# Kernel tuning notes

Measured on AMD Instinct MI355X. Metric: run time of the kernel, lower is better.

## Reference

```python
import jax, jax.numpy as jnp
import numpy as np


def _gcn_conv(x, W, b, src, dst, num_nodes):
    # PyG GCNConv: h = x @ W; symmetric normalization with self-loops; scatter-add; + bias
    h = x @ W
    deg = jax.ops.segment_sum(jnp.ones_like(dst, dtype=h.dtype), dst, num_segments=num_nodes)
    dinv = jnp.where(deg > 0, jax.lax.rsqrt(deg), 0.0)
    norm = dinv[src] * dinv[dst]                         # [E]
    msgs = h[src] * norm[:, None]                        # [E, H] gather + scale
    out = jax.ops.segment_sum(msgs, dst, num_segments=num_nodes)
    return out + b


def setup_inputs() -> dict:
    key = jax.random.key(0)
    ks = jax.random.split(key, 10)
    N, E = 500000, 1000000
    IN, H, SIG = 3, 64, 24
    x = jax.random.uniform(ks[0], (N, IN), dtype=jnp.float32)
    edge_index = jax.random.randint(ks[1], (2, E), 0, N, dtype=jnp.int64)
    batch = jnp.zeros((N,), dtype=jnp.int64)
    def glorot(k, shape):
        lim = np.sqrt(6.0 / (shape[0] + shape[1]))
        return jax.random.uniform(k, shape, dtype=jnp.float32, minval=-lim, maxval=lim)
    return {
        "x": x,
        "edge_index": edge_index,
        "batch": batch,
        "W1": glorot(ks[2], (IN, H)), "b1": jnp.zeros((H,), jnp.float32),
        "W2": glorot(ks[3], (H, H)),  "b2": jnp.zeros((H,), jnp.float32),
        "W3": glorot(ks[4], (H, H)),  "b3": jnp.zeros((H,), jnp.float32),
        "Wfc": glorot(ks[5], (H, SIG)), "bfc": jnp.zeros((SIG,), jnp.float32),
    }


def reference(x, edge_index, batch, W1, b1, W2, b2, W3, b3, Wfc, bfc):
    N = x.shape[0]
    NUM_GRAPHS = 1  # batch is all zeros (single graph)
    # add self-loops once (GCNConv adds them per layer; identical edge set each layer)
    loop = jnp.arange(N, dtype=edge_index.dtype)
    src = jnp.concatenate([edge_index[0], loop])
    dst = jnp.concatenate([edge_index[1], loop])

    h = jax.nn.relu(_gcn_conv(x, W1, b1, src, dst, N))
    h = jax.nn.relu(_gcn_conv(h, W2, b2, src, dst, N))
    h = jax.nn.relu(_gcn_conv(h, W3, b3, src, dst, N))

    # global mean pool per graph
    sums = jax.ops.segment_sum(h, batch, num_segments=NUM_GRAPHS)          # [G, H]
    counts = jax.ops.segment_sum(jnp.ones((N,), h.dtype), batch, num_segments=NUM_GRAPHS)
    sig = sums / jnp.maximum(counts, 1.0)[:, None]

    return jnp.tanh(sig @ Wfc + bfc)  # [G, 24]
```

## Files before the change

### kernel.cpp

```cpp
#include <hip/hip_runtime.h>
#include <hip/hip_bf16.h>
#include <hip/hip_fp16.h>


#define ALIGN256(x) (((x) + 255) & ~(size_t)255)
#define NBUCK_MAX 512

typedef _Float16 half8 __attribute__((ext_vector_type(8)));
typedef float f32x4 __attribute__((ext_vector_type(4)));
typedef int i32x4 __attribute__((ext_vector_type(4)));

__device__ __forceinline__ void dec16(i32x4 r, half8& a, half8& b) {
    i32x4 u, v;
    u.x = (int)(((unsigned)r.x << 8) & 0xFF00FF00u);
    u.y = (int)(((unsigned)r.x)      & 0xFF00FF00u);
    u.z = (int)(((unsigned)r.y << 8) & 0xFF00FF00u);
    u.w = (int)(((unsigned)r.y)      & 0xFF00FF00u);
    v.x = (int)(((unsigned)r.z << 8) & 0xFF00FF00u);
    v.y = (int)(((unsigned)r.z)      & 0xFF00FF00u);
    v.z = (int)(((unsigned)r.w << 8) & 0xFF00FF00u);
    v.w = (int)(((unsigned)r.w)      & 0xFF00FF00u);
    a = *(half8*)&u; b = *(half8*)&v;
}

__device__ __forceinline__ unsigned char enc8(float x) {
    unsigned short hb = __half_as_ushort(__float2half(x));
    return (unsigned char)((hb + 0x80u) >> 8);
}

__global__ __launch_bounds__(256) void init_kernel(float* __restrict__ pool, float4* __restrict__ xs,
                                                   unsigned char* __restrict__ h8a,
                                                   unsigned char* __restrict__ h8b, int N) {
    int i = threadIdx.x;
    if (i < 64) pool[i] = 0.f;
    if (i < 16) {
        ((int*)(h8a + (size_t)N * 64))[i] = 0;
        ((int*)(h8b + (size_t)N * 64))[i] = 0;
    }
    if (i == 0) xs[N] = make_float4(0.f, 0.f, 0.f, 0.f);
}

__global__ __launch_bounds__(256) void hist_kernel(const int* __restrict__ ei, int E, int CE, int SH,
                                                   int* __restrict__ cnt_mat) {
    __shared__ int h[NBUCK_MAX];
    const int t = threadIdx.x, blk = blockIdx.x;
    for (int i = t; i < NBUCK_MAX; i += 256) h[i] = 0;
    __syncthreads();
    const int e0 = blk * CE, e1 = min(E, e0 + CE);
    for (int e = e0 + t; e < e1; e += 256)
        atomicAdd(&h[ei[E + e] >> SH], 1);
    __syncthreads();
    for (int i = t; i < NBUCK_MAX; i += 256) cnt_mat[blk * NBUCK_MAX + i] = h[i];
}

__global__ __launch_bounds__(64) void colscan_kernel(const int* __restrict__ cnt_mat,
                                                     int* __restrict__ base_mat,
                                                     int* __restrict__ tot, int nblk) {
    __shared__ int ls[64];
    const int j = blockIdx.x;
    const int t = threadIdx.x;
    const int PER = (nblk + 63) >> 6;
    const int b0 = t * PER, b1 = min(nblk, b0 + PER);
    int s = 0;
    for (int b = b0; b < b1; ++b) s += cnt_mat[b * NBUCK_MAX + j];
    ls[t] = s;
    __syncthreads();
    if (t == 0) {
        int run = 0;
        for (int k = 0; k < 64; ++k) { int v = ls[k]; ls[k] = run; run += v; }
        tot[j] = run;
    }
    __syncthreads();
    int run = ls[t];
    for (int b = b0; b < b1; ++b) {
        int v = cnt_mat[b * NBUCK_MAX + j];
        base_mat[b * NBUCK_MAX + j] = run;
        run += v;
    }
}

__global__ __launch_bounds__(256) void totscan_kernel(const int* __restrict__ tot,
                                                      int* __restrict__ start, int NBK) {
    __shared__ int ls[256];
    const int t = threadIdx.x;
    const int PER = (NBK + 255) >> 8;
    const int j0 = t * PER, j1 = min(NBK, j0 + PER);
    int s = 0;
    for (int j = j0; j < j1; ++j) s += tot[j];
    ls[t] = s;
    __syncthreads();
    if (t == 0) {
        int run = 0;
        for (int k = 0; k < 256; ++k) { int v = ls[k]; ls[k] = run; run += v; }
    }
    __syncthreads();
    int run = ls[t];
    for (int j = j0; j < j1; ++j) { start[j] = run; run += tot[j]; }
}

__global__ __launch_bounds__(256) void scatter_kernel(const int* __restrict__ ei, int E, int CE, int SH,
                                                      const int* __restrict__ base_mat,
                                                      const int* __restrict__ start,
                                                      unsigned* __restrict__ bkt) {
    __shared__ int cur[NBUCK_MAX];
    const int t = threadIdx.x, blk = blockIdx.x;
    for (int i = t; i < NBUCK_MAX; i += 256) cur[i] = 0;
    __syncthreads();
    const int e0 = blk * CE, e1 = min(E, e0 + CE);
    const unsigned lowm = (1u << SH) - 1u;
    for (int e = e0 + t; e < e1; e += 256) {
        int s = ei[e], d = ei[E + e];
        int b = d >> SH;
        int r = atomicAdd(&cur[b], 1);
        int dest = start[b] + base_mat[blk * NBUCK_MAX + b] + r;
        bkt[dest] = (((unsigned)d & lowm) << 21) | (unsigned)s;
    }
}

__global__ __launch_bounds__(256) void build_kernel(const unsigned* __restrict__ bkt,
                                                    const int* __restrict__ start, const int* __restrict__ tot,
                                                    int SH, int nrows,
                                                    int* __restrict__ ell, int* __restrict__ sec) {
    __shared__ __align__(16) int loc[2048][8];
    const int t = threadIdx.x, j = blockIdx.x;
    const int R = 1 << SH;
    int4 z = make_int4(0, 0, 0, 0);
    for (int i = t; i < R * 2; i += 256) ((int4*)loc)[i] = z;
    __syncthreads();
    const int s0 = start[j], s1 = s0 + tot[j];
    for (int e = s0 + t; e < s1; e += 256) {
        unsigned p = bkt[e];
        int dl = (int)(p >> 21);
        int src = (int)(p & 0x1FFFFFu);
        int k = atomicAdd(&loc[dl][0], 1);
        if (k < 7) loc[dl][1 + k] = src;
        else if (k < 15) {
            int grow = (j << SH) + dl;
            sec[(size_t)grow * 8 + (k - 7)] = src;
        }
    }
    __syncthreads();
    const int base = j << SH;
    for (int i = t; i < R; i += 256) {
        int grow = base + i;
        if (grow < nrows) {
            int4* dst = (int4*)(ell + (size_t)grow * 8);
            dst[0] = ((int4*)&loc[i][0])[0];
            dst[1] = ((int4*)&loc[i][0])[1];
        }
    }
}

__global__ __launch_bounds__(256) void xs_kernel(const int* __restrict__ ell, const float* __restrict__ x,
                                                 float4* __restrict__ xs, int N) {
    int i = blockIdx.x * 256 + threadIdx.x;
    if (i < N) {
        float d = rsqrtf((float)(ell[(size_t)i * 8] + 1));
        xs[i] = make_float4(d * x[(size_t)i * 3 + 0], d * x[(size_t)i * 3 + 1],
                            d * x[(size_t)i * 3 + 2], 0.f);
    }
}

__global__ __launch_bounds__(256) void layer1_kernel(const float4* __restrict__ xs,
                                                     const int* __restrict__ ell,
                                                     const int* __restrict__ sec,
                                                     const float* __restrict__ W1, const float* __restrict__ b1,
                                                     unsigned char* __restrict__ hout, int N) {
    __shared__ float4 a1S[256];
    const int t = threadIdx.x;
    const int jg = blockIdx.x * 256 + t;
    const bool valid = (jg < N);
    const int jc = valid ? jg : N;

    float4 s = xs[jc];
    const int* row = ell + (size_t)(valid ? jg : 0) * 8;
    int4 e0 = *(const int4*)row;
    int4 e1 = *(const int4*)(row + 4);
    int craw = valid ? e0.x : 0;
    int deg = min(craw, 15);
    int i0 = (deg > 0) ? e0.y : N;
    int i1 = (deg > 1) ? e0.z : N;
    int i2 = (deg > 2) ? e0.w : N;
    int i3 = (deg > 3) ? e1.x : N;
    int i4 = (deg > 4) ? e1.y : N;
    int i5 = (deg > 5) ? e1.z : N;
    int i6 = (deg > 6) ? e1.w : N;
    float4 q0 = xs[i0], q1 = xs[i1], q2 = xs[i2], q3 = xs[i3];
    float4 q4 = xs[i4], q5 = xs[i5], q6 = xs[i6];
    s.x += q0.x + q1.x + q2.x + q3.x + q4.x + q5.x + q6.x;
    s.y += q0.y + q1.y + q2.y + q3.y + q4.y + q5.y + q6.y;
    s.z += q0.z + q1.z + q2.z + q3.z + q4.z + q5.z + q6.z;
    if (deg > 7) {
        const int* srow = sec + (size_t)jg * 8;
        for (int i = 7; i < deg; ++i) {
            float4 qq = xs[srow[i - 7]];
            s.x += qq.x; s.y += qq.y; s.z += qq.z;
        }
    }
    float dj = valid ? rsqrtf((float)(craw + 1)) : 0.f;
    a1S[t] = make_float4(dj * s.x, dj * s.y, dj * s.z, dj);
    __syncthreads();

    const int l = t & 63, w = t >> 6;
    const float w0 = W1[l], w1 = W1[64 + l], w2 = W1[128 + l], bl = b1[l];
    const int base = blockIdx.x * 256 + w * 64;
    #pragma unroll 4
    for (int n = 0; n < 64; ++n) {
        int j2 = base + n;
        if (j2 >= N) break;
        float4 a = a1S[w * 64 + n];
        float v = fmaf(a.x, w0, fmaf(a.y, w1, fmaf(a.z, w2, bl)));
        hout[(size_t)j2 * 64 + l] = enc8(a.w * fmaxf(v, 0.f));
    }
}

template <int POOL>
__global__ __launch_bounds__(256) void layer_kernel(const unsigned char* __restrict__ hin,
                                                    const int* __restrict__ ell,
                                                    const int* __restrict__ sec,
                                                    const float* __restrict__ W, const float* __restrict__ bias,
                                                    unsigned char* __restrict__ hout, float* __restrict__ pool, int N) {
    const int t = threadIdx.x;
    const int l = t & 63;
    const int w = t >> 6;
    const int l15 = l & 15, q = l >> 4;
    const int m = l >> 2, qq = l & 3;
    const int cbase = l & ~3;

    __shared__ float red[256];
    __shared__ __align__(16) _Float16 wlds[8 * 64 * 8];
    __shared__ __align__(16) int tbuf[4][16 * 36];

    for (int c = t; c < 512; c += 256) {
        int f = c >> 6, ln = c & 63;
        int ct = f >> 1, kt = f & 1;
        int q2 = ln >> 4, m2 = ln & 15;
        half8 b;
        #pragma unroll
        for (int j = 0; j < 8; ++j) {
            int g = 4 * q2 + (j >> 1);
            int ii = g & 7, blk = g >> 3;
            int feat = 16 * blk + 4 * (ii >> 1) + (ii & 1) + 2 * (j & 1);
            b[j] = (_Float16)W[(kt * 32 + feat) * 64 + ct * 16 + m2];
        }
        *(half8*)&wlds[(size_t)c * 8] = b;
    }
    float bb[4];
    #pragma unroll
    for (int ct = 0; ct < 4; ++ct) bb[ct] = bias[ct * 16 + l15];
    __syncthreads();

    const char* hb = (const char*)hin;
    const int vlo = qq * 16;
    float ps0 = 0.f, ps1 = 0.f, ps2 = 0.f, ps3 = 0.f;

    const int ngroups = (N + 15) >> 4;
    const int gstride = gridDim.x * 4;
    for (int g = blockIdx.x * 4 + w; g < ngroups; g += gstride) {
        const int j0 = g << 4;
        const int jm = j0 + m;
        const bool validm = (jm < N);
        const int jsm = validm ? jm : N;

        i32x4 iv = *(const i32x4*)(ell + (size_t)jsm * 8 + (qq & 1) * 4);

        int cnt = __shfl(iv.x, cbase, 64);
        int s1  = __shfl(iv.y, cbase, 64);
        int s2  = __shfl(iv.z, cbase, 64);
        int s3  = __shfl(iv.w, cbase, 64);
        int s4  = __shfl(iv.x, cbase + 1, 64);
        int s5  = __shfl(iv.y, cbase + 1, 64);
        int s6  = __shfl(iv.z, cbase + 1, 64);
        int s7  = __shfl(iv.w, cbase + 1, 64);

        int craw = validm ? cnt : 0;
        int degc = min(craw, 15);
        float djv = rsqrtf((float)(craw + 1));

        int dmax = degc;
        dmax = max(dmax, __shfl_xor(dmax, 4, 64));
        dmax = max(dmax, __shfl_xor(dmax, 8, 64));
        dmax = max(dmax, __shfl_xor(dmax, 16, 64));
        dmax = max(dmax, __shfl_xor(dmax, 32, 64));

        s1 = (degc > 0) ? s1 : N;
        s2 = (degc > 1) ? s2 : N;
        s3 = (degc > 2) ? s3 : N;
        s4 = (degc > 3) ? s4 : N;
        s5 = (degc > 4) ? s5 : N;
        s6 = (degc > 5) ? s6 : N;
        s7 = (degc > 6) ? s7 : N;

        i32x4 rS = *(const i32x4*)(hb + ((size_t)jsm << 6) + vlo);
        i32x4 r1 = *(const i32x4*)(hb + ((size_t)(unsigned)s1 << 6) + vlo);
        i32x4 r2 = *(const i32x4*)(hb + ((size_t)(unsigned)s2 << 6) + vlo);
        i32x4 r3 = *(const i32x4*)(hb + ((size_t)(unsigned)s3 << 6) + vlo);
        i32x4 r4 = *(const i32x4*)(hb + ((size_t)(unsigned)s4 << 6) + vlo);
        const bool big = (dmax > 4);
        i32x4 r5, r6, r7;
        if (big) {
            r5 = *(const i32x4*)(hb + ((size_t)(unsigned)s5 << 6) + vlo);
            r6 = *(const i32x4*)(hb + ((size_t)(unsigned)s6 << 6) + vlo);
            r7 = *(const i32x4*)(hb + ((size_t)(unsigned)s7 << 6) + vlo);
        }

        half8 aA, aB, tA, tB;
        dec16(rS, aA, aB);
        dec16(r1, tA, tB); aA += tA; aB += tB;
        dec16(r2, tA, tB); aA += tA; aB += tB;
        dec16(r3, tA, tB); aA += tA; aB += tB;
        dec16(r4, tA, tB); aA += tA; aB += tB;
        if (big) {
            dec16(r5, tA, tB); aA += tA; aB += tB;
            dec16(r6, tA, tB); aA += tA; aB += tB;
            dec16(r7, tA, tB); aA += tA; aB += tB;
        }
        if (dmax > 7) {
            const int* srow = sec + (size_t)jsm * 8;
            #pragma unroll
            for (int ww = 8; ww < 16; ++ww) {
                int sr = (degc > ww - 1) ? srow[ww - 8] : N;
                i32x4 rt = *(const i32x4*)(hb + ((size_t)(unsigned)sr << 6) + vlo);
                dec16(rt, tA, tB); aA += tA; aB += tB;
            }
        }

        *(i32x4*)&tbuf[w][m * 36 + qq * 8]     = *(i32x4*)&aA;
        *(i32x4*)&tbuf[w][m * 36 + qq * 8 + 4] = *(i32x4*)&aB;
        half8 af0 = *(half8*)&tbuf[w][l15 * 36 + 4 * q];
        half8 af1 = *(half8*)&tbuf[w][l15 * 36 + 16 + 4 * q];

        const half8* wl = (const half8*)wlds;
        f32x4 c0 = {0.f, 0.f, 0.f, 0.f}, c1 = c0, c2 = c0, c3 = c0;
        c0 = __builtin_amdgcn_mfma_f32_16x16x32_f16(af0, wl[      l], c0, 0, 0, 0);
        c1 = __builtin_amdgcn_mfma_f32_16x16x32_f16(af0, wl[128 + l], c1, 0, 0, 0);
        c2 = __builtin_amdgcn_mfma_f32_16x16x32_f16(af0, wl[256 + l], c2, 0, 0, 0);
        c3 = __builtin_amdgcn_mfma_f32_16x16x32_f16(af0, wl[384 + l], c3, 0, 0, 0);
        c0 = __builtin_amdgcn_mfma_f32_16x16x32_f16(af1, wl[ 64 + l], c0, 0, 0, 0);
        c1 = __builtin_amdgcn_mfma_f32_16x16x32_f16(af1, wl[192 + l], c1, 0, 0, 0);
        c2 = __builtin_amdgcn_mfma_f32_16x16x32_f16(af1, wl[320 + l], c2, 0, 0, 0);
        c3 = __builtin_amdgcn_mfma_f32_16x16x32_f16(af1, wl[448 + l], c3, 0, 0, 0);

        if (POOL) {
            #pragma unroll
            for (int r = 0; r < 4; ++r) {
                int row = q * 4 + r;
                int gj = j0 + row;
                float djr = __shfl(djv, row << 2, 64);
                if (gj < N) {
                    ps0 += fmaxf(djr * c0[r] + bb[0], 0.f);
                    ps1 += fmaxf(djr * c1[r] + bb[1], 0.f);
                    ps2 += fmaxf(djr * c2[r] + bb[2], 0.f);
                    ps3 += fmaxf(djr * c3[r] + bb[3], 0.f);
                }
            }
        } else {
            #pragma unroll
            for (int r = 0; r < 4; ++r) {
                int row = q * 4 + r;
                int gj = j0 + row;
                float djr = __shfl(djv, row << 2, 64);
                if (gj < N) {
                    unsigned char* hp = hout + (size_t)gj * 64 + l15;
                    hp[0]  = enc8(djr * fmaxf(djr * c0[r] + bb[0], 0.f));
                    hp[16] = enc8(djr * fmaxf(djr * c1[r] + bb[1], 0.f));
                    hp[32] = enc8(djr * fmaxf(djr * c2[r] + bb[2], 0.f));
                    hp[48] = enc8(djr * fmaxf(djr * c3[r] + bb[3], 0.f));
                }
            }
        }
    }

    if (POOL) {
        ps0 += __shfl_xor(ps0, 16, 64); ps0 += __shfl_xor(ps0, 32, 64);
        ps1 += __shfl_xor(ps1, 16, 64); ps1 += __shfl_xor(ps1, 32, 64);
        ps2 += __shfl_xor(ps2, 16, 64); ps2 += __shfl_xor(ps2, 32, 64);
        ps3 += __shfl_xor(ps3, 16, 64); ps3 += __shfl_xor(ps3, 32, 64);
        if (q == 0) {
            red[w * 64 + l15]      = ps0;
            red[w * 64 + 16 + l15] = ps1;
            red[w * 64 + 32 + l15] = ps2;
            red[w * 64 + 48 + l15] = ps3;
        }
        __syncthreads();
        if (t < 64) {
            float s = red[t] + red[64 + t] + red[128 + t] + red[192 + t];
            atomicAdd(&pool[t], s);
        }
    }
}

__global__ __launch_bounds__(64) void final_kernel(const float* __restrict__ pool, const float* __restrict__ Wfc,
                                                   const float* __restrict__ bfc, float* __restrict__ out, int N) {
    int t = threadIdx.x;
    if (t < 24) {
        float inv = 1.0f / (float)N;
        float s = bfc[t];
        for (int c = 0; c < 64; ++c) s += pool[c] * inv * Wfc[c * 24 + t];
        out[t] = tanhf(s);
    }
}

extern "C" void kernel_launch(void* const* d_in, const int* in_sizes, int n_in,
                              void* d_out, int out_size, void* d_ws, size_t ws_size,
                              hipStream_t stream) {
    const float* x   = (const float*)d_in[0];
    const int*   ei  = (const int*)d_in[1];
    const float* W1  = (const float*)d_in[3];
    const float* b1  = (const float*)d_in[4];
    const float* W2  = (const float*)d_in[5];
    const float* b2  = (const float*)d_in[6];
    const float* W3  = (const float*)d_in[7];
    const float* b3  = (const float*)d_in[8];
    const float* Wfc = (const float*)d_in[9];
    const float* bfc = (const float*)d_in[10];
    float* out = (float*)d_out;

    const int N = in_sizes[2];
    const int E = in_sizes[1] / 2;

    size_t off = 0;
    auto take = [&](size_t bytes) -> char* {
        char* p = (char*)d_ws + off;
        off = ALIGN256(off + bytes);
        return p;
    };
    const int nrows = N + 16;
    int SH = 10;
    while ((nrows >> SH) >= NBUCK_MAX) ++SH;
    const int NBK = ((nrows - 1) >> SH) + 1;
    const int CE = (E + NBK - 1) / NBK;

    int*           ell     = (int*)     take((size_t)nrows * 8 * 4);
    int*           sec     = (int*)     take((size_t)nrows * 8 * 4);
    unsigned*      bkt     = (unsigned*)take((size_t)E * 4);
    int*           cnt_mat = (int*)     take((size_t)NBUCK_MAX * NBUCK_MAX * 4);
    int*           base_mat= (int*)     take((size_t)NBUCK_MAX * NBUCK_MAX * 4);
    int*           tot     = (int*)     take(NBUCK_MAX * 4);
    int*           startb  = (int*)     take(NBUCK_MAX * 4);
    float*         pool    = (float*)   take(64 * 4);
    float4*        xs      = (float4*)  take(((size_t)N + 1) * 16);
    unsigned char* h8a     = (unsigned char*)take((size_t)(N + 1) * 64);
    unsigned char* h8b     = (unsigned char*)take((size_t)(N + 1) * 64);
    (void)ws_size; (void)n_in; (void)out_size;

    init_kernel<<<1, 256, 0, stream>>>(pool, xs, h8a, h8b, N);

    hist_kernel   <<<NBK, 256, 0, stream>>>(ei, E, CE, SH, cnt_mat);
    colscan_kernel<<<NBK,  64, 0, stream>>>(cnt_mat, base_mat, tot, NBK);
    totscan_kernel<<<1,   256, 0, stream>>>(tot, startb, NBK);
    scatter_kernel<<<NBK, 256, 0, stream>>>(ei, E, CE, SH, base_mat, startb, bkt);
    build_kernel  <<<NBK, 256, 0, stream>>>(bkt, startb, tot, SH, nrows, ell, sec);

    xs_kernel<<<(N + 255) / 256, 256, 0, stream>>>(ell, x, xs, N);

    layer1_kernel<<<(N + 255) / 256, 256, 0, stream>>>(xs, ell, sec, W1, b1, h8a, N);

    int LB = 1024;
    const int ngroups = (N + 15) >> 4;
    const int maxb = (ngroups + 3) / 4;
    if (LB > maxb) LB = maxb;

    layer_kernel<0><<<LB, 256, 0, stream>>>(h8a, ell, sec, W2, b2, h8b, nullptr, N);

    layer_kernel<1><<<LB, 256, 0, stream>>>(h8b, ell, sec, W3, b3, nullptr, pool, N);

    final_kernel<<<1, 64, 0, stream>>>(pool, Wfc, bfc, out, N);
}
```

Before: 233.9 us.

## Stage bucket scatter in LDS for coalesced writes and decouple edge chunks from buckets

The scatter kernel now builds a local histogram per edge chunk, scans it, and stages the packed edges sorted by bucket in shared memory. It then writes them to global memory in contiguous runs per bucket instead of random single-word writes. Edge chunks are now fixed at about 4096 edges, independent of the bucket count, and the minimum bucket shift rises from 10 to 11, giving fewer and larger buckets. This adds a second pass over the edge indices and more shared memory per block, which could lower occupancy. cnt_mat/base_mat are indexed by chunk with a stride of NBUCK_MAX, which assumes at most 512 chunks. E=1M gives 245 chunks, so that holds here.

```diff
diff --git a/kernel.cpp b/kernel.cpp
--- a/kernel.cpp
+++ b/kernel.cpp
@@ -102,18 +102,45 @@
                                                       const int* __restrict__ base_mat,
                                                       const int* __restrict__ start,
                                                       unsigned* __restrict__ bkt) {
+    __shared__ int sbuf[4096];
+    __shared__ unsigned short sb[4096];
+    __shared__ int lh[NBUCK_MAX];
+    __shared__ int lbase[NBUCK_MAX];
     __shared__ int cur[NBUCK_MAX];
+    __shared__ int ls[256];
     const int t = threadIdx.x, blk = blockIdx.x;
-    for (int i = t; i < NBUCK_MAX; i += 256) cur[i] = 0;
+    for (int i = t; i < NBUCK_MAX; i += 256) { lh[i] = 0; cur[i] = 0; }
     __syncthreads();
     const int e0 = blk * CE, e1 = min(E, e0 + CE);
+    for (int e = e0 + t; e < e1; e += 256)
+        atomicAdd(&lh[ei[E + e] >> SH], 1);
+    __syncthreads();
+    int a0 = lh[2 * t], a1 = lh[2 * t + 1];
+    ls[t] = a0 + a1;
+    __syncthreads();
+    if (t == 0) {
+        int run = 0;
+        for (int k = 0; k < 256; ++k) { int v = ls[k]; ls[k] = run; run += v; }
+    }
+    __syncthreads();
+    lbase[2 * t]     = ls[t];
+    lbase[2 * t + 1] = ls[t] + a0;
+    __syncthreads();
     const unsigned lowm = (1u << SH) - 1u;
     for (int e = e0 + t; e < e1; e += 256) {
         int s = ei[e], d = ei[E + e];
         int b = d >> SH;
         int r = atomicAdd(&cur[b], 1);
-        int dest = start[b] + base_mat[blk * NBUCK_MAX + b] + r;
-        bkt[dest] = (((unsigned)d & lowm) << 21) | (unsigned)s;
+        int slot = lbase[b] + r;
+        sbuf[slot] = (int)((((unsigned)d & lowm) << 21) | (unsigned)s);
+        sb[slot] = (unsigned short)b;
+    }
+    __syncthreads();
+    const int n = e1 - e0;
+    for (int i = t; i < n; i += 256) {
+        int b = sb[i];
+        int dest = start[b] + base_mat[blk * NBUCK_MAX + b] + (i - lbase[b]);
+        bkt[dest] = (unsigned)sbuf[i];
     }
 }
 
@@ -426,10 +453,11 @@
         return p;
     };
     const int nrows = N + 16;
-    int SH = 10;
-    while ((nrows >> SH) >= NBUCK_MAX) ++SH;
+    int SH = 11;
+    while ((((nrows - 1) >> SH) + 1) > NBUCK_MAX) ++SH;
     const int NBK = ((nrows - 1) >> SH) + 1;
-    const int CE = (E + NBK - 1) / NBK;
+    const int NCHUNK = (E + 4095) / 4096;
+    const int CE = (E + NCHUNK - 1) / NCHUNK;
 
     int*           ell     = (int*)     take((size_t)nrows * 8 * 4);
     int*           sec     = (int*)     take((size_t)nrows * 8 * 4);
@@ -446,11 +474,11 @@
 
     init_kernel<<<1, 256, 0, stream>>>(pool, xs, h8a, h8b, N);
 
-    hist_kernel   <<<NBK, 256, 0, stream>>>(ei, E, CE, SH, cnt_mat);
-    colscan_kernel<<<NBK,  64, 0, stream>>>(cnt_mat, base_mat, tot, NBK);
-    totscan_kernel<<<1,   256, 0, stream>>>(tot, startb, NBK);
-    scatter_kernel<<<NBK, 256, 0, stream>>>(ei, E, CE, SH, base_mat, startb, bkt);
-    build_kernel  <<<NBK, 256, 0, stream>>>(bkt, startb, tot, SH, nrows, ell, sec);
+    hist_kernel   <<<NCHUNK, 256, 0, stream>>>(ei, E, CE, SH, cnt_mat);
+    colscan_kernel<<<NBK,     64, 0, stream>>>(cnt_mat, base_mat, tot, NCHUNK);
+    totscan_kernel<<<1,      256, 0, stream>>>(tot, startb, NBK);
+    scatter_kernel<<<NCHUNK, 256, 0, stream>>>(ei, E, CE, SH, base_mat, startb, bkt);
+    build_kernel  <<<NBK,    256, 0, stream>>>(bkt, startb, tot, SH, nrows, ell, sec);
 
     xs_kernel<<<(N + 255) / 256, 256, 0, stream>>>(ell, x, xs, N);
 
```

Result: no change. 234.2 us (+0.1%).
